# Optimization experiments

Hardware: AMD Instinct MI355X
Metric: run time of the kernel (lower is better)

Reference implementation:

```python
import jax, jax.numpy as jnp
import numpy as np
from jax import lax

D_MODEL = 2048
D_STATE = 16
D_CONV = 4
B_SZ = 2
T_LEN = 2048


def setup_inputs() -> dict:
    key = jax.random.key(0)
    ks = jax.random.split(key, 8)
    x = jax.random.normal(ks[0], (B_SZ, T_LEN, D_MODEL), dtype=jnp.float32)
    h = jnp.zeros((B_SZ, D_MODEL, D_STATE), dtype=jnp.float32)
    norm_w = jnp.ones((D_MODEL,), dtype=jnp.float32)
    in_proj_w = jax.random.normal(ks[1], (2 * D_MODEL, D_MODEL), dtype=jnp.float32) * (D_MODEL ** -0.5)
    conv_w = jax.random.normal(ks[2], (D_MODEL, 1, D_CONV), dtype=jnp.float32) * 0.5
    conv_b = jnp.zeros((D_MODEL,), dtype=jnp.float32)
    x_proj_w = jax.random.normal(ks[3], (D_MODEL + 2 * D_STATE, D_MODEL), dtype=jnp.float32) * (D_MODEL ** -0.5)
    A_log = jnp.broadcast_to(jnp.log(jnp.arange(1, D_STATE + 1, dtype=jnp.float32))[None, :], (D_MODEL, D_STATE)).copy()
    D = jnp.ones((D_MODEL,), dtype=jnp.float32)
    out_proj_w = jax.random.normal(ks[4], (D_MODEL, D_MODEL), dtype=jnp.float32) * (D_MODEL ** -0.5)
    return {"x": x, "h": h, "norm_w": norm_w, "in_proj_w": in_proj_w,
            "conv_w": conv_w, "conv_b": conv_b, "x_proj_w": x_proj_w,
            "A_log": A_log, "D": D, "out_proj_w": out_proj_w}


def _rmsnorm(x, w, eps=1e-6):
    ms = jnp.mean(jnp.square(x.astype(jnp.float32)), axis=-1, keepdims=True)
    return (x * lax.rsqrt(ms + eps).astype(x.dtype)) * w.astype(x.dtype)


def reference(x, h, norm_w, in_proj_w, conv_w, conv_b, x_proj_w, A_log, D, out_proj_w):
    B, T, d_model = x.shape
    d_state = A_log.shape[1]
    residual = x
    x_normed = _rmsnorm(x, norm_w)
    xz = x_normed @ in_proj_w.T                      # (B, T, 2*d_model)
    x_branch, z = jnp.split(xz, 2, axis=-1)
    # depthwise causal conv1d: torch pads both sides by d_conv-1 then slices [:T],
    # equivalent to left-pad-only causal conv.
    xc = x_branch.transpose(0, 2, 1)                 # (B, d_model, T)
    xc = lax.conv_general_dilated(
        xc, conv_w, window_strides=(1,), padding=[(D_CONV - 1, 0)],
        dimension_numbers=("NCH", "OIH", "NCH"), feature_group_count=d_model)
    xc = xc + conv_b[None, :, None]
    x_ssm = jax.nn.silu(xc.transpose(0, 2, 1))       # (B, T, d_model)

    # SSM core
    proj = x_ssm @ x_proj_w.T                        # (B, T, d_model + 2*d_state)
    delta_raw = proj[..., :d_model]
    B_in = proj[..., d_model:d_model + d_state]
    C_in = proj[..., d_model + d_state:]
    delta = jax.nn.softplus(delta_raw)               # (B, T, d_model)
    A = -jnp.exp(A_log.astype(jnp.float32))          # (d_model, d_state)

    def step(h_c, inp):
        d_t, b_t, c_t, x_t = inp                     # (B,dm) (B,ds) (B,ds) (B,dm)
        A_bar = jnp.exp(d_t[:, :, None] * A[None])   # (B, dm, ds)
        h_c = A_bar * h_c + (d_t * x_t)[:, :, None] * b_t[:, None, :]
        y_t = jnp.einsum("bdn,bn->bd", h_c, c_t) + D * x_t
        return h_c, y_t

    xs = (delta.transpose(1, 0, 2), B_in.transpose(1, 0, 2),
          C_in.transpose(1, 0, 2), x_ssm.transpose(1, 0, 2))
    h_new, ys = lax.scan(step, h.astype(x.dtype), xs)
    y = ys.transpose(1, 0, 2)                        # (B, T, d_model)

    y = y * jax.nn.silu(z)
    out = residual + y @ out_proj_w.T
    return out, lax.stop_gradient(h_new)
```

## Files before the change

kernel.cpp:

```cpp
#include <hip/hip_runtime.h>
#include <cstdint>
#include <cstddef>


typedef __bf16 bf16_t;
typedef __attribute__((ext_vector_type(8))) __bf16 bf16x8;
typedef __attribute__((ext_vector_type(4))) __bf16 bf16x4;
typedef __attribute__((ext_vector_type(4))) float f32x4;

#define D_MODEL 2048
#define D_STATE 16
#define B_SZ 2
#define T_LEN 2048
#define N_ROWS (B_SZ * T_LEN)
#define N_PAD  2176
#define N_CHUNK 32
#define L_CHUNK (T_LEN / N_CHUNK)
#define LOG2E 1.4426950408889634f

__device__ __forceinline__ void load_lds16(const void* g, void* l) {
    __builtin_amdgcn_global_load_lds(
        (const __attribute__((address_space(1))) void*)(uintptr_t)g,
        (__attribute__((address_space(3))) void*)(uintptr_t)l,
        16, 0, 0);
}

__global__ __launch_bounds__(256) void cast_w13(
    const float* __restrict__ w1, const float* __restrict__ w3,
    bf16_t* __restrict__ d1, bf16_t* __restrict__ d3)
{
    int i = blockIdx.x * 256 + threadIdx.x;
    const int n1 = 4096 * 2048 / 4;
    if (i < n1) {
        f32x4 v = ((const f32x4*)w1)[i];
        ((bf16x4*)d1)[i] = __builtin_convertvector(v, bf16x4);
    } else {
        int j = i - n1;
        f32x4 v = ((const f32x4*)w3)[j];
        ((bf16x4*)d3)[j] = __builtin_convertvector(v, bf16x4);
    }
}

__global__ __launch_bounds__(256) void cast_pad_w2(
    const float* __restrict__ s, bf16_t* __restrict__ d)
{
    int i = blockIdx.x * 256 + threadIdx.x;
    int row = i >> 11;
    int col = i & 2047;
    float v = (row < 2080) ? s[(size_t)row * 2048 + col] : 0.f;
    d[i] = (bf16_t)v;
}

__global__ __launch_bounds__(256) void rmsnorm_kernel(
    const float* __restrict__ x, const float* __restrict__ w,
    bf16_t* __restrict__ xn)
{
    int row = blockIdx.x;
    int tid = threadIdx.x;
    const float* xr = x + (size_t)row * D_MODEL;
    float ss = 0.f;
    for (int i = tid; i < D_MODEL; i += 256) { float v = xr[i]; ss = fmaf(v, v, ss); }
    #pragma unroll
    for (int o = 32; o > 0; o >>= 1) ss += __shfl_down(ss, o, 64);
    __shared__ float red[4];
    if ((tid & 63) == 0) red[tid >> 6] = ss;
    __syncthreads();
    float tot = red[0] + red[1] + red[2] + red[3];
    float scale = rsqrtf(tot * (1.f / D_MODEL) + 1e-6f);
    bf16_t* xo = xn + (size_t)row * D_MODEL;
    for (int i = tid; i < D_MODEL; i += 256) xo[i] = (bf16_t)(xr[i] * scale * w[i]);
}

template<int MODE>
__global__ __launch_bounds__(256) void gemm_bt(
    const bf16_t* __restrict__ A, const bf16_t* __restrict__ B, int K,
    float* __restrict__ out0, bf16_t* __restrict__ out1,
    const float* __restrict__ add)
{
    __shared__ __align__(16) bf16_t lA[128 * 32];
    __shared__ __align__(16) bf16_t lB[128 * 32];
    __shared__ __align__(16) float cs[32 * 132];
    const int tid = threadIdx.x;
    const int bm = blockIdx.x, bn = blockIdx.y;

    const int rA = tid >> 2;
    const int cA = (tid & 3) * 8;
    const bf16_t* aSrc = A + ((size_t)bm * 128 + rA) * K + cA;
    const bf16_t* bSrc = B + ((size_t)bn * 128 + rA) * K + cA;

    const int lane = tid & 63;
    const int wave = tid >> 6;
    const int wm = (wave & 1) * 64;
    const int wn = (wave >> 1) * 64;
    const int fr = lane & 15;
    const int quad = lane >> 4;
    const int aOff = (wm + fr) * 32 + quad * 8;
    const int bOff = (wn + fr) * 32 + quad * 8;

    f32x4 acc[4][4];
    #pragma unroll
    for (int i = 0; i < 4; ++i)
        #pragma unroll
        for (int j = 0; j < 4; ++j) acc[i][j] = {0.f, 0.f, 0.f, 0.f};

    const int kIters = K >> 5;
    for (int kt = 0; kt < kIters; ++kt) {
        load_lds16(aSrc,                  &lA[tid * 8]);
        load_lds16(aSrc + (size_t)64 * K, &lA[2048 + tid * 8]);
        load_lds16(bSrc,                  &lB[tid * 8]);
        load_lds16(bSrc + (size_t)64 * K, &lB[2048 + tid * 8]);
        aSrc += 32; bSrc += 32;
        __syncthreads();

        bf16x8 af[4], bv[4];
        #pragma unroll
        for (int i = 0; i < 4; ++i) af[i] = *(const bf16x8*)(&lA[aOff + i * 512]);
        #pragma unroll
        for (int j = 0; j < 4; ++j) bv[j] = *(const bf16x8*)(&lB[bOff + j * 512]);
        #pragma unroll
        for (int i = 0; i < 4; ++i)
            #pragma unroll
            for (int j = 0; j < 4; ++j)
                acc[i][j] = __builtin_amdgcn_mfma_f32_16x16x32_bf16(
                    af[i], bv[j], acc[i][j], 0, 0, 0);
        __syncthreads();
    }

    const int lrow0 = (wave & 1) * 16 + quad * 4;
    const int lcol0 = wn + fr;
    for (int i = 0; i < 4; ++i) {
        __syncthreads();
        #pragma unroll
        for (int j = 0; j < 4; ++j)
            #pragma unroll
            for (int rr = 0; rr < 4; ++rr)
                cs[(lrow0 + rr) * 132 + lcol0 + j * 16] = acc[i][j][rr];
        __syncthreads();
        #pragma unroll
        for (int k = 0; k < 4; ++k) {
            int f4  = tid + k * 256;
            int row = f4 >> 5;
            int c4  = (f4 & 31) * 4;
            f32x4 v = *(const f32x4*)&cs[row * 132 + c4];
            int gr = bm * 128 + i * 16 + ((row < 16) ? row : (48 + row));
            int gc = bn * 128 + c4;
            if (MODE == 0) {
                if (bn < 16) {
                    *(f32x4*)&out0[(size_t)gr * 2048 + gc] = v;
                } else {
                    bf16x4 o;
                    #pragma unroll
                    for (int e = 0; e < 4; ++e) {
                        float s = v[e];
                        o[e] = (bf16_t)(s / (1.f + __expf(-s)));
                    }
                    *(bf16x4*)&out1[(size_t)gr * 2048 + (gc - 2048)] = o;
                }
            } else if (MODE == 1) {
                if (bn < 16) {
                    #pragma unroll
                    for (int e = 0; e < 4; ++e) {
                        float s = v[e];
                        v[e] = fmaxf(s, 0.f) + __logf(1.f + __expf(-fabsf(s)));
                    }
                }
                *(f32x4*)&out0[(size_t)gr * N_PAD + gc] = v;
            } else {
                f32x4 a4 = *(const f32x4*)&add[(size_t)gr * 2048 + gc];
                v = v + a4;
                *(f32x4*)&out0[(size_t)gr * 2048 + gc] = v;
            }
        }
    }
}

__global__ __launch_bounds__(256) void conv_silu_kernel(
    const float* __restrict__ xb, const float* __restrict__ cw,
    const float* __restrict__ cb, bf16_t* __restrict__ xs_b)
{
    int id = blockIdx.x * 256 + threadIdx.x;
    int d  = id & 2047;
    int tb = (id >> 11) & 255;
    int b  = id >> 19;
    float w0 = cw[d * 4 + 0], w1 = cw[d * 4 + 1], w2 = cw[d * 4 + 2], w3 = cw[d * 4 + 3];
    float bias = cb[d];
    int t0 = tb * 8;
    size_t base = (size_t)b * T_LEN;
    float v[11];
    #pragma unroll
    for (int i = 0; i < 11; ++i) {
        int t = t0 - 3 + i;
        v[i] = (t >= 0) ? xb[(base + t) * 2048 + d] : 0.f;
    }
    #pragma unroll
    for (int j = 0; j < 8; ++j) {
        float s = bias + w0 * v[j] + w1 * v[j + 1] + w2 * v[j + 2] + w3 * v[j + 3];
        float sl = s / (1.f + __expf(-s));
        xs_b[(base + t0 + j) * D_MODEL + d] = (bf16_t)sl;
    }
}

#define PF 4

__global__ __launch_bounds__(256) void scan_phase1(
    const float* __restrict__ proj, const bf16_t* __restrict__ xs,
    const float* __restrict__ A_log,
    float* __restrict__ Aprod, float* __restrict__ hfin)
{
    int wi   = blockIdx.x * 4 + (threadIdx.x >> 6);
    int lane = threadIdx.x & 63;
    int nq   = lane & 3;
    int dsub = lane >> 2;
    int c  = wi & 31;
    int dg = (wi >> 5) & 127;
    int b  = wi >> 12;
    int dd = dg * 16 + dsub;

    float A2[4], h[4], Ap[4];
    #pragma unroll
    for (int j = 0; j < 4; ++j) {
        A2[j] = -__expf(A_log[dd * D_STATE + nq * 4 + j]) * LOG2E;
        h[j] = 0.f; Ap[j] = 1.f;
    }
    const int t0 = c * L_CHUNK;
    const int tmax = t0 + L_CHUNK - 1;

    float p_da[PF], p_xv[PF];
    f32x4 p_B[PF];
    #pragma unroll
    for (int u = 0; u < PF; ++u) {
        size_t row = (size_t)b * T_LEN + t0 + u;
        const float* pr = proj + row * N_PAD;
        p_da[u] = pr[dd];
        p_xv[u] = (float)xs[row * D_MODEL + dd];
        p_B[u]  = *(const f32x4*)(pr + D_MODEL + nq * 4);
    }

    for (int it = 0; it < L_CHUNK; it += PF) {
        #pragma unroll
        for (int u = 0; u < PF; ++u) {
            int t = t0 + it + u;
            float da = p_da[u], xv = p_xv[u];
            f32x4 Bv = p_B[u];
            int tn = t + PF; tn = (tn > tmax) ? tmax : tn;
            {
                size_t row = (size_t)b * T_LEN + tn;
                const float* pr = proj + row * N_PAD;
                p_da[u] = pr[dd];
                p_xv[u] = (float)xs[row * D_MODEL + dd];
                p_B[u]  = *(const f32x4*)(pr + D_MODEL + nq * 4);
            }
            float dx = da * xv;
            #pragma unroll
            for (int j = 0; j < 4; ++j) {
                float a = exp2f(da * A2[j]);
                Ap[j] *= a;
                h[j] = fmaf(a, h[j], dx * Bv[j]);
            }
        }
    }
    size_t o = ((size_t)c * 4096 + b * 2048 + dd) * D_STATE + nq * 4;
    *(f32x4*)(Aprod + o) = f32x4{Ap[0], Ap[1], Ap[2], Ap[3]};
    *(f32x4*)(hfin  + o) = f32x4{h[0], h[1], h[2], h[3]};
}

__global__ __launch_bounds__(256) void scan_phase2(
    const float* __restrict__ h_in, const float* __restrict__ Aprod,
    float* __restrict__ hfin, float* __restrict__ h_out)
{
    int g = blockIdx.x * 256 + threadIdx.x;
    float h = h_in[g];
    for (int c = 0; c < N_CHUNK; ++c) {
        size_t o = (size_t)c * 65536 + g;
        float a   = Aprod[o];
        float loc = hfin[o];
        hfin[o] = h;
        h = fmaf(a, h, loc);
    }
    h_out[g] = h;
}

__global__ __launch_bounds__(256) void scan_phase3(
    const float* __restrict__ proj, const bf16_t* __restrict__ xs,
    const bf16_t* __restrict__ zg, const float* __restrict__ A_log,
    const float* __restrict__ Dv, const float* __restrict__ hinit,
    bf16_t* __restrict__ yg)
{
    int wi   = blockIdx.x * 4 + (threadIdx.x >> 6);
    int lane = threadIdx.x & 63;
    int nq   = lane & 3;
    int dsub = lane >> 2;
    int c  = wi & 31;
    int dg = (wi >> 5) & 127;
    int b  = wi >> 12;
    int dd = dg * 16 + dsub;

    float A2[4], h[4];
    size_t o = ((size_t)c * 4096 + b * 2048 + dd) * D_STATE + nq * 4;
    #pragma unroll
    for (int j = 0; j < 4; ++j) {
        A2[j] = -__expf(A_log[dd * D_STATE + nq * 4 + j]) * LOG2E;
        h[j]  = hinit[o + j];
    }
    float Dd = Dv[dd];
    const int t0 = c * L_CHUNK;
    const int tmax = t0 + L_CHUNK - 1;

    float p_da[PF], p_xv[PF], p_sz[PF];
    f32x4 p_B[PF], p_C[PF];
    #pragma unroll
    for (int u = 0; u < PF; ++u) {
        size_t row = (size_t)b * T_LEN + t0 + u;
        const float* pr = proj + row * N_PAD;
        p_da[u] = pr[dd];
        p_xv[u] = (float)xs[row * D_MODEL + dd];
        p_sz[u] = (float)zg[row * 2048 + dd];
        p_B[u]  = *(const f32x4*)(pr + D_MODEL + nq * 4);
        p_C[u]  = *(const f32x4*)(pr + D_MODEL + D_STATE + nq * 4);
    }

    for (int it = 0; it < L_CHUNK; it += PF) {
        #pragma unroll
        for (int u = 0; u < PF; ++u) {
            int t = t0 + it + u;
            float da = p_da[u], xv = p_xv[u], sz = p_sz[u];
            f32x4 Bv = p_B[u], Cv = p_C[u];
            int tn = t + PF; tn = (tn > tmax) ? tmax : tn;
            {
                size_t row = (size_t)b * T_LEN + tn;
                const float* pr = proj + row * N_PAD;
                p_da[u] = pr[dd];
                p_xv[u] = (float)xs[row * D_MODEL + dd];
                p_sz[u] = (float)zg[row * 2048 + dd];
                p_B[u]  = *(const f32x4*)(pr + D_MODEL + nq * 4);
                p_C[u]  = *(const f32x4*)(pr + D_MODEL + D_STATE + nq * 4);
            }
            float dx = da * xv;
            float yp = 0.f;
            #pragma unroll
            for (int j = 0; j < 4; ++j) {
                float a = exp2f(da * A2[j]);
                h[j] = fmaf(a, h[j], dx * Bv[j]);
                yp = fmaf(h[j], Cv[j], yp);
            }
            yp += __shfl_xor(yp, 1, 64);
            yp += __shfl_xor(yp, 2, 64);
            if (nq == 0) {
                float y = fmaf(Dd, xv, yp);
                yg[((size_t)b * T_LEN + t) * D_MODEL + dd] = (bf16_t)(y * sz);
            }
        }
    }
}

extern "C" void kernel_launch(void* const* d_in, const int* in_sizes, int n_in,
                              void* d_out, int out_size, void* d_ws, size_t ws_size,
                              hipStream_t stream)
{
    const float* x    = (const float*)d_in[0];
    const float* h0   = (const float*)d_in[1];
    const float* nw   = (const float*)d_in[2];
    const float* w_in = (const float*)d_in[3];
    const float* cw   = (const float*)d_in[4];
    const float* cb   = (const float*)d_in[5];
    const float* w_x  = (const float*)d_in[6];
    const float* alog = (const float*)d_in[7];
    const float* dv   = (const float*)d_in[8];
    const float* w_out= (const float*)d_in[9];
    float* out  = (float*)d_out;
    float* hout = out + (size_t)N_ROWS * D_MODEL;

    char* ws = (char*)d_ws;
    size_t off = 0;
    auto alloc = [&](size_t bytes) -> void* {
        void* p = ws + off;
        off += (bytes + 255) & ~(size_t)255;
        return p;
    };
    bf16_t* W1  = (bf16_t*)alloc((size_t)4096 * 2048 * 2);
    bf16_t* W2  = (bf16_t*)alloc((size_t)N_PAD * 2048 * 2);
    bf16_t* W3  = (bf16_t*)alloc((size_t)2048 * 2048 * 2);
    bf16_t* XN  = (bf16_t*)alloc((size_t)N_ROWS * 2048 * 2);
    float*  XB  = (float*) alloc((size_t)N_ROWS * 2048 * 4);
    bf16_t* ZG  = (bf16_t*)alloc((size_t)N_ROWS * 2048 * 2);
    float*  PROJ= (float*) alloc((size_t)N_ROWS * N_PAD * 4);
    float* APROD= (float*) alloc((size_t)N_CHUNK * 4096 * D_STATE * 4);
    float* HFIN = (float*) alloc((size_t)N_CHUNK * 4096 * D_STATE * 4);
    bf16_t* XSb = W1;
    bf16_t* YG  = XN;

    cast_w13<<<(4096 * 2048 / 4 + 2048 * 2048 / 4) / 256, 256, 0, stream>>>(w_in, w_out, W1, W3);
    cast_pad_w2<<<(N_PAD * 2048) / 256, 256, 0, stream>>>(w_x, W2);

    rmsnorm_kernel<<<N_ROWS, 256, 0, stream>>>(x, nw, XN);
    gemm_bt<0><<<dim3(32, 32), 256, 0, stream>>>(XN, W1, 2048, XB, ZG, nullptr);
    conv_silu_kernel<<<(B_SZ * (T_LEN / 8) * D_MODEL) / 256, 256, 0, stream>>>(XB, cw, cb, XSb);
    gemm_bt<1><<<dim3(32, N_PAD / 128), 256, 0, stream>>>(XSb, W2, 2048, PROJ, nullptr, nullptr);
    scan_phase1<<<2048, 256, 0, stream>>>(PROJ, XSb, alog, APROD, HFIN);
    scan_phase2<<<256, 256, 0, stream>>>(h0, APROD, HFIN, hout);
    scan_phase3<<<2048, 256, 0, stream>>>(PROJ, XSb, ZG, alog, dv, HFIN, YG);
    gemm_bt<2><<<dim3(32, 16), 256, 0, stream>>>(YG, W3, 2048, out, nullptr, x);

    (void)in_sizes; (void)n_in; (void)out_size; (void)ws_size;
}
```

Baseline: 525.3 us.

## Store GEMM operands in MFMA-fragment swizzled layout and drop LDS staging

Weights and activations (normed x, conv output, gated y) are now written in a pre-swizzled 16x32 tile layout matching the MFMA fragment order. The GEMM then loads fragments directly from global memory into registers with one-step prefetch, removing LDS staging and the per-iteration barriers. Producers and the scan kernels are changed to read and write this layout, and the weight casts are merged into one kernel. The risk is that each wave fetches its operands from global or cache on its own, with no sharing of tiles through LDS across the block, so it relies on cache reuse and latency hiding from the register prefetch.

```diff
diff --git a/kernel.cpp b/kernel.cpp
--- a/kernel.cpp
+++ b/kernel.cpp
@@ -17,85 +17,103 @@
 #define N_CHUNK 32
 #define L_CHUNK (T_LEN / N_CHUNK)
 #define LOG2E 1.4426950408889634f
-
-__device__ __forceinline__ void load_lds16(const void* g, void* l) {
-    __builtin_amdgcn_global_load_lds(
-        (const __attribute__((address_space(1))) void*)(uintptr_t)g,
-        (__attribute__((address_space(3))) void*)(uintptr_t)l,
-        16, 0, 0);
-}
-
-__global__ __launch_bounds__(256) void cast_w13(
-    const float* __restrict__ w1, const float* __restrict__ w3,
-    bf16_t* __restrict__ d1, bf16_t* __restrict__ d3)
-{
-    int i = blockIdx.x * 256 + threadIdx.x;
-    const int n1 = 4096 * 2048 / 4;
-    if (i < n1) {
-        f32x4 v = ((const f32x4*)w1)[i];
-        ((bf16x4*)d1)[i] = __builtin_convertvector(v, bf16x4);
-    } else {
-        int j = i - n1;
-        f32x4 v = ((const f32x4*)w3)[j];
-        ((bf16x4*)d3)[j] = __builtin_convertvector(v, bf16x4);
-    }
-}
-
-__global__ __launch_bounds__(256) void cast_pad_w2(
-    const float* __restrict__ s, bf16_t* __restrict__ d)
-{
-    int i = blockIdx.x * 256 + threadIdx.x;
-    int row = i >> 11;
-    int col = i & 2047;
-    float v = (row < 2080) ? s[(size_t)row * 2048 + col] : 0.f;
-    d[i] = (bf16_t)v;
-}
-
-__global__ __launch_bounds__(256) void rmsnorm_kernel(
+#define KT 64
+#define PANEL 32768
+
+__device__ __forceinline__ size_t swz_idx(int row, int col) {
+    return ((size_t)((row >> 4) * KT + (col >> 5)) << 9)
+         + (size_t)(((row & 15) + (((col & 31) >> 3) << 4)) << 3) + (col & 7);
+}
+
+__global__ __launch_bounds__(256) void cast_weights(
+    const float* __restrict__ w_in, const float* __restrict__ w_x,
+    const float* __restrict__ w_out,
+    bf16_t* __restrict__ W1s, bf16_t* __restrict__ W2s, bf16_t* __restrict__ W3s)
+{
+    int wv   = blockIdx.x * 4 + (threadIdx.x >> 6);
+    int lane = threadIdx.x & 63;
+    const float* src; bf16_t* dst; int nrows; int tile;
+    if (wv < 16384)      { src = w_in;  dst = W1s; tile = wv;         nrows = 4096; }
+    else if (wv < 25088) { src = w_x;   dst = W2s; tile = wv - 16384; nrows = 2080; }
+    else                 { src = w_out; dst = W3s; tile = wv - 25088; nrows = 2048; }
+    int r16 = tile >> 6, kt = tile & 63;
+    int row = r16 * 16 + (lane & 15);
+    int k0  = kt * 32 + (lane >> 4) * 8;
+    f32x4 v0 = {0.f, 0.f, 0.f, 0.f}, v1 = v0;
+    if (row < nrows) {
+        v0 = *(const f32x4*)&src[(size_t)row * 2048 + k0];
+        v1 = *(const f32x4*)&src[(size_t)row * 2048 + k0 + 4];
+    }
+    bf16x4 lo = __builtin_convertvector(v0, bf16x4);
+    bf16x4 hi = __builtin_convertvector(v1, bf16x4);
+    bf16x8 o;
+    #pragma unroll
+    for (int e = 0; e < 4; ++e) { o[e] = lo[e]; o[e + 4] = hi[e]; }
+    *(bf16x8*)(dst + (size_t)tile * 512 + lane * 8) = o;
+}
+
+__global__ __launch_bounds__(256) void rmsnorm_swz(
     const float* __restrict__ x, const float* __restrict__ w,
     bf16_t* __restrict__ xn)
 {
-    int row = blockIdx.x;
+    int r16 = blockIdx.x;
     int tid = threadIdx.x;
-    const float* xr = x + (size_t)row * D_MODEL;
-    float ss = 0.f;
-    for (int i = tid; i < D_MODEL; i += 256) { float v = xr[i]; ss = fmaf(v, v, ss); }
-    #pragma unroll
-    for (int o = 32; o > 0; o >>= 1) ss += __shfl_down(ss, o, 64);
-    __shared__ float red[4];
-    if ((tid & 63) == 0) red[tid >> 6] = ss;
+    int wave = tid >> 6, lane = tid & 63;
+    __shared__ float sc[16];
+    #pragma unroll
+    for (int rr = 0; rr < 4; ++rr) {
+        int row = r16 * 16 + wave * 4 + rr;
+        const float* xr = x + (size_t)row * 2048;
+        float ss = 0.f;
+        for (int i = lane * 4; i < 2048; i += 256) {
+            f32x4 v = *(const f32x4*)&xr[i];
+            ss += v[0]*v[0] + v[1]*v[1] + v[2]*v[2] + v[3]*v[3];
+        }
+        #pragma unroll
+        for (int o = 32; o > 0; o >>= 1) ss += __shfl_down(ss, o, 64);
+        if (lane == 0) sc[wave * 4 + rr] = rsqrtf(ss * (1.f / 2048.f) + 1e-6f);
+    }
     __syncthreads();
-    float tot = red[0] + red[1] + red[2] + red[3];
-    float scale = rsqrtf(tot * (1.f / D_MODEL) + 1e-6f);
-    bf16_t* xo = xn + (size_t)row * D_MODEL;
-    for (int i = tid; i < D_MODEL; i += 256) xo[i] = (bf16_t)(xr[i] * scale * w[i]);
+    const size_t base = (size_t)r16 * PANEL;
+    int m = lane & 15;
+    int row = r16 * 16 + m;
+    float s = sc[m];
+    const float* xr = x + (size_t)row * 2048;
+    for (int c = 0; c < 16; ++c) {
+        int f  = (c * 256 + tid) * 8;
+        int kt = f >> 9;
+        int k  = kt * 32 + (lane >> 4) * 8;
+        f32x4 v0 = *(const f32x4*)&xr[k];
+        f32x4 v1 = *(const f32x4*)&xr[k + 4];
+        f32x4 w0 = *(const f32x4*)&w[k];
+        f32x4 w1 = *(const f32x4*)&w[k + 4];
+        bf16x8 o;
+        #pragma unroll
+        for (int e = 0; e < 4; ++e) {
+            o[e]     = (bf16_t)(v0[e] * s * w0[e]);
+            o[e + 4] = (bf16_t)(v1[e] * s * w1[e]);
+        }
+        *(bf16x8*)(xn + base + f) = o;
+    }
 }
 
 template<int MODE>
 __global__ __launch_bounds__(256) void gemm_bt(
-    const bf16_t* __restrict__ A, const bf16_t* __restrict__ B, int K,
+    const bf16_t* __restrict__ A, const bf16_t* __restrict__ B,
     float* __restrict__ out0, bf16_t* __restrict__ out1,
     const float* __restrict__ add)
 {
-    __shared__ __align__(16) bf16_t lA[128 * 32];
-    __shared__ __align__(16) bf16_t lB[128 * 32];
     __shared__ __align__(16) float cs[32 * 132];
     const int tid = threadIdx.x;
     const int bm = blockIdx.x, bn = blockIdx.y;
-
-    const int rA = tid >> 2;
-    const int cA = (tid & 3) * 8;
-    const bf16_t* aSrc = A + ((size_t)bm * 128 + rA) * K + cA;
-    const bf16_t* bSrc = B + ((size_t)bn * 128 + rA) * K + cA;
-
     const int lane = tid & 63;
     const int wave = tid >> 6;
-    const int wm = (wave & 1) * 64;
     const int wn = (wave >> 1) * 64;
     const int fr = lane & 15;
     const int quad = lane >> 4;
-    const int aOff = (wm + fr) * 32 + quad * 8;
-    const int bOff = (wn + fr) * 32 + quad * 8;
+
+    const bf16_t* aB = A + (((size_t)(bm * 8 + (wave & 1) * 4) * KT) << 9) + lane * 8;
+    const bf16_t* bB = B + (((size_t)(bn * 8 + (wave >> 1) * 4) * KT) << 9) + lane * 8;
 
     f32x4 acc[4][4];
     #pragma unroll
@@ -103,27 +121,29 @@
         #pragma unroll
         for (int j = 0; j < 4; ++j) acc[i][j] = {0.f, 0.f, 0.f, 0.f};
 
-    const int kIters = K >> 5;
-    for (int kt = 0; kt < kIters; ++kt) {
-        load_lds16(aSrc,                  &lA[tid * 8]);
-        load_lds16(aSrc + (size_t)64 * K, &lA[2048 + tid * 8]);
-        load_lds16(bSrc,                  &lB[tid * 8]);
-        load_lds16(bSrc + (size_t)64 * K, &lB[2048 + tid * 8]);
-        aSrc += 32; bSrc += 32;
-        __syncthreads();
-
-        bf16x8 af[4], bv[4];
-        #pragma unroll
-        for (int i = 0; i < 4; ++i) af[i] = *(const bf16x8*)(&lA[aOff + i * 512]);
-        #pragma unroll
-        for (int j = 0; j < 4; ++j) bv[j] = *(const bf16x8*)(&lB[bOff + j * 512]);
+    bf16x8 aC[4], bC[4];
+    #pragma unroll
+    for (int i = 0; i < 4; ++i) {
+        aC[i] = *(const bf16x8*)(aB + (size_t)i * PANEL);
+        bC[i] = *(const bf16x8*)(bB + (size_t)i * PANEL);
+    }
+    #pragma unroll 2
+    for (int kt = 0; kt < KT; ++kt) {
+        const int ktn = (kt < KT - 1) ? (kt + 1) : (KT - 1);
+        bf16x8 aN[4], bN[4];
+        #pragma unroll
+        for (int i = 0; i < 4; ++i) {
+            aN[i] = *(const bf16x8*)(aB + (size_t)i * PANEL + ((size_t)ktn << 9));
+            bN[i] = *(const bf16x8*)(bB + (size_t)i * PANEL + ((size_t)ktn << 9));
+        }
         #pragma unroll
         for (int i = 0; i < 4; ++i)
             #pragma unroll
             for (int j = 0; j < 4; ++j)
                 acc[i][j] = __builtin_amdgcn_mfma_f32_16x16x32_bf16(
-                    af[i], bv[j], acc[i][j], 0, 0, 0);
-        __syncthreads();
+                    aC[i], bC[j], acc[i][j], 0, 0, 0);
+        #pragma unroll
+        for (int i = 0; i < 4; ++i) { aC[i] = aN[i]; bC[i] = bN[i]; }
     }
 
     const int lrow0 = (wave & 1) * 16 + quad * 4;
@@ -174,33 +194,54 @@
     }
 }
 
-__global__ __launch_bounds__(256) void conv_silu_kernel(
+__global__ __launch_bounds__(256) void conv_silu_swz(
     const float* __restrict__ xb, const float* __restrict__ cw,
-    const float* __restrict__ cb, bf16_t* __restrict__ xs_b)
+    const float* __restrict__ cb, bf16_t* __restrict__ xs_s)
 {
     int id = blockIdx.x * 256 + threadIdx.x;
-    int d  = id & 2047;
-    int tb = (id >> 11) & 255;
+    int dq = id & 255;
+    int t  = (id >> 8) & 2047;
     int b  = id >> 19;
-    float w0 = cw[d * 4 + 0], w1 = cw[d * 4 + 1], w2 = cw[d * 4 + 2], w3 = cw[d * 4 + 3];
-    float bias = cb[d];
-    int t0 = tb * 8;
-    size_t base = (size_t)b * T_LEN;
-    float v[11];
-    #pragma unroll
-    for (int i = 0; i < 11; ++i) {
-        int t = t0 - 3 + i;
-        v[i] = (t >= 0) ? xb[(base + t) * 2048 + d] : 0.f;
-    }
-    #pragma unroll
-    for (int j = 0; j < 8; ++j) {
-        float s = bias + w0 * v[j] + w1 * v[j + 1] + w2 * v[j + 2] + w3 * v[j + 3];
-        float sl = s / (1.f + __expf(-s));
-        xs_b[(base + t0 + j) * D_MODEL + d] = (bf16_t)sl;
-    }
+    int d0 = dq * 8;
+    f32x4 cwv[8];
+    #pragma unroll
+    for (int e = 0; e < 8; ++e) cwv[e] = *(const f32x4*)&cw[(d0 + e) * 4];
+    float a[8];
+    {
+        f32x4 b0 = *(const f32x4*)&cb[d0], b1 = *(const f32x4*)&cb[d0 + 4];
+        #pragma unroll
+        for (int e = 0; e < 4; ++e) { a[e] = b0[e]; a[4 + e] = b1[e]; }
+    }
+    #pragma unroll
+    for (int tap = 0; tap < 4; ++tap) {
+        int tr = t - 3 + tap;
+        if (tr >= 0) {
+            const float* xr = xb + ((size_t)(b * 2048 + tr)) * 2048 + d0;
+            f32x4 x0 = *(const f32x4*)xr, x1 = *(const f32x4*)(xr + 4);
+            #pragma unroll
+            for (int e = 0; e < 4; ++e) {
+                a[e]     = fmaf(cwv[e][tap],     x0[e], a[e]);
+                a[4 + e] = fmaf(cwv[4 + e][tap], x1[e], a[4 + e]);
+            }
+        }
+    }
+    bf16x8 o;
+    #pragma unroll
+    for (int e = 0; e < 8; ++e) {
+        float s = a[e];
+        o[e] = (bf16_t)(s / (1.f + __expf(-s)));
+    }
+    int row = b * 2048 + t;
+    size_t off = ((size_t)((row >> 4) * KT + (dq >> 2)) << 9)
+               + (size_t)(((row & 15) + ((dq & 3) << 4)) << 3);
+    *(bf16x8*)(xs_s + off) = o;
 }
 
 #define PF 4
+
+__device__ __forceinline__ size_t xs_off(int row, int ddo) {
+    return ((size_t)(row >> 4) << 15) + (size_t)((row & 15) << 3) + ddo;
+}
 
 __global__ __launch_bounds__(256) void scan_phase1(
     const float* __restrict__ proj, const bf16_t* __restrict__ xs,
@@ -215,6 +256,7 @@
     int dg = (wi >> 5) & 127;
     int b  = wi >> 12;
     int dd = dg * 16 + dsub;
+    const int ddo = ((dd >> 5) << 9) + (((dd & 31) >> 3) << 7) + (dd & 7);
 
     float A2[4], h[4], Ap[4];
     #pragma unroll
@@ -229,10 +271,10 @@
     f32x4 p_B[PF];
     #pragma unroll
     for (int u = 0; u < PF; ++u) {
-        size_t row = (size_t)b * T_LEN + t0 + u;
-        const float* pr = proj + row * N_PAD;
+        int row = b * T_LEN + t0 + u;
+        const float* pr = proj + (size_t)row * N_PAD;
         p_da[u] = pr[dd];
-        p_xv[u] = (float)xs[row * D_MODEL + dd];
+        p_xv[u] = (float)xs[xs_off(row, ddo)];
         p_B[u]  = *(const f32x4*)(pr + D_MODEL + nq * 4);
     }
 
@@ -244,10 +286,10 @@
             f32x4 Bv = p_B[u];
             int tn = t + PF; tn = (tn > tmax) ? tmax : tn;
             {
-                size_t row = (size_t)b * T_LEN + tn;
-                const float* pr = proj + row * N_PAD;
+                int row = b * T_LEN + tn;
+                const float* pr = proj + (size_t)row * N_PAD;
                 p_da[u] = pr[dd];
-                p_xv[u] = (float)xs[row * D_MODEL + dd];
+                p_xv[u] = (float)xs[xs_off(row, ddo)];
                 p_B[u]  = *(const f32x4*)(pr + D_MODEL + nq * 4);
             }
             float dx = da * xv;
@@ -294,6 +336,7 @@
     int dg = (wi >> 5) & 127;
     int b  = wi >> 12;
     int dd = dg * 16 + dsub;
+    const int ddo = ((dd >> 5) << 9) + (((dd & 31) >> 3) << 7) + (dd & 7);
 
     float A2[4], h[4];
     size_t o = ((size_t)c * 4096 + b * 2048 + dd) * D_STATE + nq * 4;
@@ -310,11 +353,11 @@
     f32x4 p_B[PF], p_C[PF];
     #pragma unroll
     for (int u = 0; u < PF; ++u) {
-        size_t row = (size_t)b * T_LEN + t0 + u;
-        const float* pr = proj + row * N_PAD;
+        int row = b * T_LEN + t0 + u;
+        const float* pr = proj + (size_t)row * N_PAD;
         p_da[u] = pr[dd];
-        p_xv[u] = (float)xs[row * D_MODEL + dd];
-        p_sz[u] = (float)zg[row * 2048 + dd];
+        p_xv[u] = (float)xs[xs_off(row, ddo)];
+        p_sz[u] = (float)zg[(size_t)row * 2048 + dd];
         p_B[u]  = *(const f32x4*)(pr + D_MODEL + nq * 4);
         p_C[u]  = *(const f32x4*)(pr + D_MODEL + D_STATE + nq * 4);
     }
@@ -327,11 +370,11 @@
             f32x4 Bv = p_B[u], Cv = p_C[u];
             int tn = t + PF; tn = (tn > tmax) ? tmax : tn;
             {
-                size_t row = (size_t)b * T_LEN + tn;
-                const float* pr = proj + row * N_PAD;
+                int row = b * T_LEN + tn;
+                const float* pr = proj + (size_t)row * N_PAD;
                 p_da[u] = pr[dd];
-                p_xv[u] = (float)xs[row * D_MODEL + dd];
-                p_sz[u] = (float)zg[row * 2048 + dd];
+                p_xv[u] = (float)xs[xs_off(row, ddo)];
+                p_sz[u] = (float)zg[(size_t)row * 2048 + dd];
                 p_B[u]  = *(const f32x4*)(pr + D_MODEL + nq * 4);
                 p_C[u]  = *(const f32x4*)(pr + D_MODEL + D_STATE + nq * 4);
             }
@@ -347,7 +390,8 @@
             yp += __shfl_xor(yp, 2, 64);
             if (nq == 0) {
                 float y = fmaf(Dd, xv, yp);
-                yg[((size_t)b * T_LEN + t) * D_MODEL + dd] = (bf16_t)(y * sz);
+                int row = b * T_LEN + t;
+                yg[xs_off(row, ddo)] = (bf16_t)(y * sz);
             }
         }
     }
@@ -377,9 +421,9 @@
         off += (bytes + 255) & ~(size_t)255;
         return p;
     };
-    bf16_t* W1  = (bf16_t*)alloc((size_t)4096 * 2048 * 2);
-    bf16_t* W2  = (bf16_t*)alloc((size_t)N_PAD * 2048 * 2);
-    bf16_t* W3  = (bf16_t*)alloc((size_t)2048 * 2048 * 2);
+    bf16_t* W1  = (bf16_t*)alloc((size_t)16384 * 512 * 2);
+    bf16_t* W2  = (bf16_t*)alloc((size_t)8704 * 512 * 2);
+    bf16_t* W3  = (bf16_t*)alloc((size_t)8192 * 512 * 2);
     bf16_t* XN  = (bf16_t*)alloc((size_t)N_ROWS * 2048 * 2);
     float*  XB  = (float*) alloc((size_t)N_ROWS * 2048 * 4);
     bf16_t* ZG  = (bf16_t*)alloc((size_t)N_ROWS * 2048 * 2);
@@ -389,17 +433,16 @@
     bf16_t* XSb = W1;
     bf16_t* YG  = XN;
 
-    cast_w13<<<(4096 * 2048 / 4 + 2048 * 2048 / 4) / 256, 256, 0, stream>>>(w_in, w_out, W1, W3);
-    cast_pad_w2<<<(N_PAD * 2048) / 256, 256, 0, stream>>>(w_x, W2);
-
-    rmsnorm_kernel<<<N_ROWS, 256, 0, stream>>>(x, nw, XN);
-    gemm_bt<0><<<dim3(32, 32), 256, 0, stream>>>(XN, W1, 2048, XB, ZG, nullptr);
-    conv_silu_kernel<<<(B_SZ * (T_LEN / 8) * D_MODEL) / 256, 256, 0, stream>>>(XB, cw, cb, XSb);
-    gemm_bt<1><<<dim3(32, N_PAD / 128), 256, 0, stream>>>(XSb, W2, 2048, PROJ, nullptr, nullptr);
+    cast_weights<<<8320, 256, 0, stream>>>(w_in, w_x, w_out, W1, W2, W3);
+
+    rmsnorm_swz<<<256, 256, 0, stream>>>(x, nw, XN);
+    gemm_bt<0><<<dim3(32, 32), 256, 0, stream>>>(XN, W1, XB, ZG, nullptr);
+    conv_silu_swz<<<(B_SZ * T_LEN * 256) / 256, 256, 0, stream>>>(XB, cw, cb, XSb);
+    gemm_bt<1><<<dim3(32, N_PAD / 128), 256, 0, stream>>>(XSb, W2, PROJ, nullptr, nullptr);
     scan_phase1<<<2048, 256, 0, stream>>>(PROJ, XSb, alog, APROD, HFIN);
     scan_phase2<<<256, 256, 0, stream>>>(h0, APROD, HFIN, hout);
     scan_phase3<<<2048, 256, 0, stream>>>(PROJ, XSb, ZG, alog, dv, HFIN, YG);
-    gemm_bt<2><<<dim3(32, 16), 256, 0, stream>>>(YG, W3, 2048, out, nullptr, x);
+    gemm_bt<2><<<dim3(32, 16), 256, 0, stream>>>(YG, W3, out, nullptr, x);
 
     (void)in_sizes; (void)n_in; (void)out_size; (void)ws_size;
 }
```

New measurement: 541.9 us. 1.03x slower.
